# Performance work log

Measured on AMD Instinct MI355X. Metric: run time of the kernel, lower is better.

The kernel has to match this reference:

```python
import jax, jax.numpy as jnp
import numpy as np

N_CAMS, B, J, H, W = 5, 4, 15, 128, 240
CUBE = (80, 80, 20)
NBINS = CUBE[0] * CUBE[1] * CUBE[2]
EPS = 1e-6


def setup_inputs() -> dict:
    key = jax.random.key(0)
    ks = jax.random.split(key, 8)
    heatmaps = jax.random.uniform(ks[0], (N_CAMS, B, J, H, W), dtype=jnp.float32)
    # cameras: rotations about z, placed so scene depth is positive
    ang = np.linspace(0.0, 2 * np.pi, N_CAMS, endpoint=False)
    Rz = np.stack([np.stack([np.cos(ang), -np.sin(ang), np.zeros(N_CAMS)], -1),
                   np.stack([np.sin(ang), np.cos(ang), np.zeros(N_CAMS)], -1),
                   np.stack([np.zeros(N_CAMS), np.zeros(N_CAMS), np.ones(N_CAMS)], -1)], 1)  # [N,3,3]
    R = jnp.asarray(np.broadcast_to(Rz[:, None], (N_CAMS, B, 3, 3)), dtype=jnp.float32)
    T = jnp.broadcast_to(jnp.asarray([0.0, 0.0, -5000.0], jnp.float32), (N_CAMS, B, 3))
    f = jnp.full((N_CAMS, B, 2), 1000.0, jnp.float32)
    c = jnp.broadcast_to(jnp.asarray([960.0, 540.0], jnp.float32), (N_CAMS, B, 2))
    k = 0.01 * jax.random.normal(ks[1], (N_CAMS, B, 3), dtype=jnp.float32)
    p = 0.001 * jax.random.normal(ks[2], (N_CAMS, B, 2), dtype=jnp.float32)
    image_wh = jnp.broadcast_to(jnp.asarray([1920.0, 1080.0], jnp.float32), (N_CAMS, B, 2))
    grid_center = jnp.asarray([0.0, 0.0, 1000.0], jnp.float32) + \
        50.0 * jax.random.normal(ks[3], (B, 3), dtype=jnp.float32)
    grid_size = jnp.asarray([8000.0, 8000.0, 2000.0], jnp.float32)
    return {"heatmaps": heatmaps, "R": R, "T": T, "f": f, "c": c, "k": k,
            "p": p, "image_wh": image_wh, "grid_center": grid_center,
            "grid_size": grid_size}


def compute_grid(grid_size, center):
    # torch.meshgrid default == indexing='ij'
    ax = [jnp.linspace(-grid_size[i] / 2, grid_size[i] / 2, CUBE[i]) + center[i]
          for i in range(3)]
    gx, gy, gz = jnp.meshgrid(ax[0], ax[1], ax[2], indexing='ij')
    return jnp.stack([gx.ravel(), gy.ravel(), gz.ravel()], axis=1)  # [NBINS,3]


def _bilinear_sample(img, g):
    # img [J,H,W]; g [M,2] normalized coords (x,y), align_corners=True, zero pad
    ix = (g[:, 0] + 1.0) * 0.5 * (W - 1)
    iy = (g[:, 1] + 1.0) * 0.5 * (H - 1)
    x0 = jnp.floor(ix); y0 = jnp.floor(iy)
    x1 = x0 + 1.0; y1 = y0 + 1.0
    wx1 = ix - x0; wx0 = 1.0 - wx1
    wy1 = iy - y0; wy0 = 1.0 - wy1

    def gather(xi, yi):
        valid = ((xi >= 0) & (xi < W) & (yi >= 0) & (yi < H)).astype(img.dtype)
        xc = jnp.clip(xi, 0, W - 1).astype(jnp.int32)
        yc = jnp.clip(yi, 0, H - 1).astype(jnp.int32)
        return img[:, yc, xc] * valid  # [J,M]

    return (gather(x0, y0) * (wx0 * wy0) + gather(x1, y0) * (wx1 * wy0) +
            gather(x0, y1) * (wx0 * wy1) + gather(x1, y1) * (wx1 * wy1))


def reference(heatmaps, R, T, f, c, k, p, image_wh, grid_center, grid_size):
    # world grids per sample: [B, NBINS, 3]
    grids = jax.vmap(lambda ctr: compute_grid(grid_size, ctr))(grid_center)
    # project: xcam = R @ (x - T)
    d = grids[None] - T[:, :, None, :]                      # [N,B,M,3]
    xcam = jnp.einsum('nbij,nbmj->nbmi', R, d)              # [N,B,M,3]
    y = xcam[..., :2] / xcam[..., 2:3]                      # [N,B,M,2]
    r2 = jnp.sum(y * y, axis=-1)                            # [N,B,M]
    radial = 1.0 + k[:, :, None, 0] * r2 + k[:, :, None, 1] * r2**2 \
                 + k[:, :, None, 2] * r2**3
    tan = p[:, :, None, 0] * y[..., 1] + p[:, :, None, 1] * y[..., 0]
    xy = y * (radial + tan)[..., None] + \
        r2[..., None] * jnp.stack([p[..., 1], p[..., 0]], -1)[:, :, None, :]
    pix = xy * f[:, :, None, :] + c[:, :, None, :]          # [N,B,M,2]

    wv = image_wh[:, :, None, 0]
    hv = image_wh[:, :, None, 1]
    bound = ((pix[..., 0] >= 0) & (pix[..., 1] >= 0) &
             (pix[..., 0] < wv) & (pix[..., 1] < hv)).astype(heatmaps.dtype)  # [N,B,M]
    maxwh = jnp.maximum(wv, hv)[..., None]
    pixc = jnp.clip(pix, -1.0, maxwh)
    norm = pixc / (image_wh[:, :, None, :] - 1.0) * 2.0 - 1.0
    norm = jnp.clip(norm, -1.1, 1.1)                        # [N,B,M,2]

    sampled = jax.vmap(jax.vmap(_bilinear_sample))(heatmaps, norm)  # [N,B,J,M]

    num = jnp.sum(sampled * bound[:, :, None, :], axis=0)   # [B,J,M]
    den = jnp.sum(bound, axis=0)[:, None, :] + EPS          # [B,1,M]
    cubes = num / den
    cubes = jnp.where(jnp.isnan(cubes), 0.0, cubes)
    cubes = jnp.clip(cubes, 0.0, 1.0)
    cubes = cubes.reshape(B, J, *CUBE)
    return cubes, grids
```

## Files before the change

### kernel.cpp

```cpp
#include <hip/hip_runtime.h>

#define NCAMS 5
#define BB 4
#define JJ 15
#define HH 128
#define WW 240
#define CXX 80
#define CYY 80
#define CZZ 20
#define NBINS 128000
#define HW (HH*WW)
#define CUBES_ELEMS (BB*JJ*NBINS)
#define BLOCK 256
#define BLOCKS_PER_B (NBINS / BLOCK)
#define GRID (BB * BLOCKS_PER_B)
#define WS_NEEDED ((size_t)NCAMS * BB * HW * 16)

__device__ __forceinline__ unsigned prm(unsigned a, unsigned b, unsigned s) {
#if __has_builtin(__builtin_amdgcn_perm)
    return __builtin_amdgcn_perm(a, b, s);
#else
    unsigned long long v = ((unsigned long long)a << 32) | b;
    unsigned r = 0;
#pragma unroll
    for (int i = 0; i < 4; ++i) {
        unsigned idx = (s >> (8 * i)) & 0xffu;
        unsigned byte = (idx < 8) ? (unsigned)((v >> (8 * idx)) & 0xff) : 0u;
        r |= byte << (8 * i);
    }
    return r;
#endif
}

__device__ __forceinline__ unsigned dot4u8(unsigned a, unsigned b, unsigned c) {
#if __has_builtin(__builtin_amdgcn_udot4)
    return __builtin_amdgcn_udot4(a, b, c, false);
#else
    return c + (a & 0xff) * (b & 0xff)
             + ((a >> 8) & 0xff) * ((b >> 8) & 0xff)
             + ((a >> 16) & 0xff) * ((b >> 16) & 0xff)
             + (a >> 24) * (b >> 24);
#endif
}

__global__ __launch_bounds__(BLOCK) void transpose_kernel_u8(
    const float* __restrict__ hm, uint4* __restrict__ tz)
{
    const int t = blockIdx.x * BLOCK + threadIdx.x;
    const int nb = t / HW;
    const int pix = t - nb * HW;
    const float* src = hm + (size_t)nb * JJ * HW + pix;
    unsigned w[4] = {0u, 0u, 0u, 0u};
#pragma unroll
    for (int j = 0; j < JJ; ++j) {
        const float v = src[j * HW];
        unsigned u = (unsigned)(v * 255.f + 0.5f);
        u = u > 255u ? 255u : u;
        w[j >> 2] |= u << ((j & 3) * 8);
    }
    uint4 o; o.x = w[0]; o.y = w[1]; o.z = w[2]; o.w = w[3];
    tz[t] = o;
}

__global__ __launch_bounds__(BLOCK) void project_kernel_u8(
    const uint4* __restrict__ tz,
    const float* __restrict__ R, const float* __restrict__ T,
    const float* __restrict__ f, const float* __restrict__ c,
    const float* __restrict__ k, const float* __restrict__ p,
    const float* __restrict__ wh,
    const float* __restrict__ gc, const float* __restrict__ gs,
    float* __restrict__ out)
{
    const int tile = ((blockIdx.x & 7) * (GRID / 8)) + (blockIdx.x >> 3);
    const int b = tile / BLOCKS_PER_B;
    const int m = (tile % BLOCKS_PER_B) * BLOCK + threadIdx.x;

    const int i   = m / (CYY * CZZ);
    const int rem = m - i * (CYY * CZZ);
    const int jy  = rem / CZZ;
    const int kz  = rem - jy * CZZ;

    const float gs0 = gs[0], gs1 = gs[1], gs2 = gs[2];
    const float gx = -0.5f * gs0 + (float)i  * (gs0 / (float)(CXX - 1)) + gc[b * 3 + 0];
    const float gy = -0.5f * gs1 + (float)jy * (gs1 / (float)(CYY - 1)) + gc[b * 3 + 1];
    const float gz = -0.5f * gs2 + (float)kz * (gs2 / (float)(CZZ - 1)) + gc[b * 3 + 2];

    float* gout = out + CUBES_ELEMS + ((size_t)b * NBINS + m) * 3;
    gout[0] = gx; gout[1] = gy; gout[2] = gz;

    unsigned acc[JJ];
#pragma unroll
    for (int j = 0; j < JJ; ++j) acc[j] = 0u;
    float den = 0.f;

    for (int n = 0; n < NCAMS; ++n) {
        const int pb = n * BB + b;
        const float* Rp = R + pb * 9;

        const float dx = gx - T[pb * 3 + 0];
        const float dy = gy - T[pb * 3 + 1];
        const float dz = gz - T[pb * 3 + 2];

        const float xc = Rp[0] * dx + Rp[1] * dy + Rp[2] * dz;
        const float yc = Rp[3] * dx + Rp[4] * dy + Rp[5] * dz;
        const float zc = Rp[6] * dx + Rp[7] * dy + Rp[8] * dz;

        const float y0 = xc / zc;
        const float y1 = yc / zc;
        const float r2 = y0 * y0 + y1 * y1;

        const float k0 = k[pb * 3 + 0], k1 = k[pb * 3 + 1], k2 = k[pb * 3 + 2];
        const float radial = 1.f + k0 * r2 + k1 * r2 * r2 + k2 * r2 * r2 * r2;
        const float p0v = p[pb * 2 + 0], p1v = p[pb * 2 + 1];
        const float s = radial + p0v * y1 + p1v * y0;
        const float xy0 = y0 * s + r2 * p1v;
        const float xy1 = y1 * s + r2 * p0v;

        const float pixx = xy0 * f[pb * 2 + 0] + c[pb * 2 + 0];
        const float pixy = xy1 * f[pb * 2 + 1] + c[pb * 2 + 1];

        const float wv = wh[pb * 2 + 0], hv = wh[pb * 2 + 1];
        const bool inb = (pixx >= 0.f) & (pixy >= 0.f) & (pixx < wv) & (pixy < hv);
        if (!inb) continue;
        den += 1.f;

        const float maxwh = fmaxf(wv, hv);
        float pcx = fminf(fmaxf(pixx, -1.f), maxwh);
        float pcy = fminf(fmaxf(pixy, -1.f), maxwh);
        float nx = fminf(fmaxf(pcx / (wv - 1.f) * 2.f - 1.f, -1.1f), 1.1f);
        float ny = fminf(fmaxf(pcy / (hv - 1.f) * 2.f - 1.f, -1.1f), 1.1f);

        const float ix = (nx + 1.f) * 0.5f * (float)(WW - 1);
        const float iy = (ny + 1.f) * 0.5f * (float)(HH - 1);
        const float x0f = floorf(ix), y0f = floorf(iy);
        const float x1f = x0f + 1.f, y1f = y0f + 1.f;
        const float wx1 = ix - x0f, wx0 = 1.f - wx1;
        const float wy1 = iy - y0f, wy0 = 1.f - wy1;

        const float vx0 = (x0f >= 0.f && x0f < (float)WW) ? 1.f : 0.f;
        const float vx1 = (x1f >= 0.f && x1f < (float)WW) ? 1.f : 0.f;
        const float vy0 = (y0f >= 0.f && y0f < (float)HH) ? 1.f : 0.f;
        const float vy1 = (y1f >= 0.f && y1f < (float)HH) ? 1.f : 0.f;

        const float w00 = wx0 * wy0 * vx0 * vy0;
        const float w10 = wx1 * wy0 * vx1 * vy0;
        const float w01 = wx0 * wy1 * vx0 * vy1;
        const float w11 = wx1 * wy1 * vx1 * vy1;

        const int xi0 = min(max((int)x0f, 0), WW - 1);
        const int xi1 = min(max((int)x1f, 0), WW - 1);
        const int yi0 = min(max((int)y0f, 0), HH - 1);
        const int yi1 = min(max((int)y1f, 0), HH - 1);

        const uint4* img = tz + (size_t)pb * HW;
        const uint4 A = img[yi0 * WW + xi0];
        const uint4 Bc = img[yi0 * WW + xi1];
        const uint4 Cc = img[yi1 * WW + xi0];
        const uint4 D = img[yi1 * WW + xi1];

        const unsigned u00 = (unsigned)(w00 * 255.f + 0.5f);
        const unsigned u10 = (unsigned)(w10 * 255.f + 0.5f);
        const unsigned u01 = (unsigned)(w01 * 255.f + 0.5f);
        const unsigned u11 = (unsigned)(w11 * 255.f + 0.5f);
        const unsigned wp = u00 | (u10 << 8) | (u01 << 16) | (u11 << 24);

        const unsigned Aa[4] = {A.x,  A.y,  A.z,  A.w};
        const unsigned Ba[4] = {Bc.x, Bc.y, Bc.z, Bc.w};
        const unsigned Ca[4] = {Cc.x, Cc.y, Cc.z, Cc.w};
        const unsigned Da[4] = {D.x,  D.y,  D.z,  D.w};

#pragma unroll
        for (int j = 0; j < JJ; ++j) {
            const int d = j >> 2;
            const unsigned bj = (unsigned)(j & 3);
            const unsigned selAB = 0x0c0c0000u | (bj << 8) | (bj + 4u);
            const unsigned mAB = prm(Aa[d], Ba[d], selAB);
            const unsigned mCD = prm(Ca[d], Da[d], selAB);
            const unsigned bytes = prm(mAB, mCD, 0x01000504u);
            acc[j] = dot4u8(bytes, wp, acc[j]);
        }
    }

    const float inv = 1.f / ((den + 1e-6f) * (255.f * 255.f));
    float* cout = out + (size_t)b * JJ * NBINS + m;
#pragma unroll
    for (int j = 0; j < JJ; ++j) {
        float v = (float)acc[j] * inv;
        v = fminf(fmaxf(v, 0.f), 1.f);
        cout[(size_t)j * NBINS] = v;
    }
}

__global__ __launch_bounds__(BLOCK) void project_kernel_fb(
    const float* __restrict__ hm,
    const float* __restrict__ R, const float* __restrict__ T,
    const float* __restrict__ f, const float* __restrict__ c,
    const float* __restrict__ k, const float* __restrict__ p,
    const float* __restrict__ wh,
    const float* __restrict__ gc, const float* __restrict__ gs,
    float* __restrict__ out)
{
    const int b = blockIdx.x / BLOCKS_PER_B;
    const int m = (blockIdx.x % BLOCKS_PER_B) * BLOCK + threadIdx.x;
    const int i   = m / (CYY * CZZ);
    const int rem = m - i * (CYY * CZZ);
    const int jy  = rem / CZZ;
    const int kz  = rem - jy * CZZ;

    const float gs0 = gs[0], gs1 = gs[1], gs2 = gs[2];
    const float gx = -0.5f * gs0 + (float)i  * (gs0 / (float)(CXX - 1)) + gc[b * 3 + 0];
    const float gy = -0.5f * gs1 + (float)jy * (gs1 / (float)(CYY - 1)) + gc[b * 3 + 1];
    const float gz = -0.5f * gs2 + (float)kz * (gs2 / (float)(CZZ - 1)) + gc[b * 3 + 2];

    float* gout = out + CUBES_ELEMS + ((size_t)b * NBINS + m) * 3;
    gout[0] = gx; gout[1] = gy; gout[2] = gz;

    float num[JJ];
#pragma unroll
    for (int j = 0; j < JJ; ++j) num[j] = 0.f;
    float den = 0.f;

    for (int n = 0; n < NCAMS; ++n) {
        const int pb = n * BB + b;
        const float* Rp = R + pb * 9;
        const float dx = gx - T[pb * 3 + 0];
        const float dy = gy - T[pb * 3 + 1];
        const float dz = gz - T[pb * 3 + 2];
        const float xc = Rp[0] * dx + Rp[1] * dy + Rp[2] * dz;
        const float yc = Rp[3] * dx + Rp[4] * dy + Rp[5] * dz;
        const float zc = Rp[6] * dx + Rp[7] * dy + Rp[8] * dz;
        const float y0 = xc / zc;
        const float y1 = yc / zc;
        const float r2 = y0 * y0 + y1 * y1;
        const float k0 = k[pb * 3 + 0], k1 = k[pb * 3 + 1], k2 = k[pb * 3 + 2];
        const float radial = 1.f + k0 * r2 + k1 * r2 * r2 + k2 * r2 * r2 * r2;
        const float p0v = p[pb * 2 + 0], p1v = p[pb * 2 + 1];
        const float s = radial + p0v * y1 + p1v * y0;
        const float xy0 = y0 * s + r2 * p1v;
        const float xy1 = y1 * s + r2 * p0v;
        const float pixx = xy0 * f[pb * 2 + 0] + c[pb * 2 + 0];
        const float pixy = xy1 * f[pb * 2 + 1] + c[pb * 2 + 1];
        const float wv = wh[pb * 2 + 0], hv = wh[pb * 2 + 1];
        const bool inb = (pixx >= 0.f) & (pixy >= 0.f) & (pixx < wv) & (pixy < hv);
        if (!inb) continue;
        den += 1.f;
        const float maxwh = fmaxf(wv, hv);
        float pcx = fminf(fmaxf(pixx, -1.f), maxwh);
        float pcy = fminf(fmaxf(pixy, -1.f), maxwh);
        float nx = fminf(fmaxf(pcx / (wv - 1.f) * 2.f - 1.f, -1.1f), 1.1f);
        float ny = fminf(fmaxf(pcy / (hv - 1.f) * 2.f - 1.f, -1.1f), 1.1f);
        const float ix = (nx + 1.f) * 0.5f * (float)(WW - 1);
        const float iy = (ny + 1.f) * 0.5f * (float)(HH - 1);
        const float x0f = floorf(ix), y0f = floorf(iy);
        const float x1f = x0f + 1.f, y1f = y0f + 1.f;
        const float wx1 = ix - x0f, wx0 = 1.f - wx1;
        const float wy1 = iy - y0f, wy0 = 1.f - wy1;
        const float vx0 = (x0f >= 0.f && x0f < (float)WW) ? 1.f : 0.f;
        const float vx1 = (x1f >= 0.f && x1f < (float)WW) ? 1.f : 0.f;
        const float vy0 = (y0f >= 0.f && y0f < (float)HH) ? 1.f : 0.f;
        const float vy1 = (y1f >= 0.f && y1f < (float)HH) ? 1.f : 0.f;
        const float w00 = wx0 * wy0 * vx0 * vy0;
        const float w10 = wx1 * wy0 * vx1 * vy0;
        const float w01 = wx0 * wy1 * vx0 * vy1;
        const float w11 = wx1 * wy1 * vx1 * vy1;
        const int xi0 = min(max((int)x0f, 0), WW - 1);
        const int xi1 = min(max((int)x1f, 0), WW - 1);
        const int yi0 = min(max((int)y0f, 0), HH - 1);
        const int yi1 = min(max((int)y1f, 0), HH - 1);
        const int o00 = yi0 * WW + xi0;
        const int o10 = yi0 * WW + xi1;
        const int o01 = yi1 * WW + xi0;
        const int o11 = yi1 * WW + xi1;
        const float* img = hm + (size_t)pb * JJ * HW;
#pragma unroll
        for (int j = 0; j < JJ; ++j) {
            const float* pj = img + j * HW;
            num[j] += pj[o00] * w00 + pj[o10] * w10 + pj[o01] * w01 + pj[o11] * w11;
        }
    }

    const float inv = 1.f / (den + 1e-6f);
    float* cout = out + (size_t)b * JJ * NBINS + m;
#pragma unroll
    for (int j = 0; j < JJ; ++j) {
        float v = num[j] * inv;
        v = (v != v) ? 0.f : v;
        v = fminf(fmaxf(v, 0.f), 1.f);
        cout[(size_t)j * NBINS] = v;
    }
}

extern "C" void kernel_launch(void* const* d_in, const int* in_sizes, int n_in,
                              void* d_out, int out_size, void* d_ws, size_t ws_size,
                              hipStream_t stream) {
    const float* hm = (const float*)d_in[0];
    const float* R  = (const float*)d_in[1];
    const float* T  = (const float*)d_in[2];
    const float* f  = (const float*)d_in[3];
    const float* c  = (const float*)d_in[4];
    const float* k  = (const float*)d_in[5];
    const float* p  = (const float*)d_in[6];
    const float* wh = (const float*)d_in[7];
    const float* gc = (const float*)d_in[8];
    const float* gs = (const float*)d_in[9];
    float* out = (float*)d_out;

    if (ws_size >= WS_NEEDED) {
        uint4* tz = (uint4*)d_ws;
        transpose_kernel_u8<<<dim3(NCAMS * BB * HW / BLOCK), dim3(BLOCK), 0, stream>>>(
            hm, tz);
        project_kernel_u8<<<dim3(GRID), dim3(BLOCK), 0, stream>>>(
            tz, R, T, f, c, k, p, wh, gc, gs, out);
    } else {
        project_kernel_fb<<<dim3(GRID), dim3(BLOCK), 0, stream>>>(
            hm, R, T, f, c, k, p, wh, gc, gs, out);
    }
}
```

Baseline: 119.9 us.

## Use nontemporal memory ops, branchless camera loop, and shared byte-transpose permutes

Heatmap loads in the transpose kernel and the cube and grid output stores now use nontemporal hints, which keeps streaming data from polluting the cache. The camera loop is fully unrolled and made branchless: out-of-bounds cameras zero the packed weights instead of skipping the iteration, which removes divergence but always issues the four gathers. The per-joint 3-permute byte extraction becomes a 4x4 byte transpose per dword that shares intermediate permutes, cutting permute instructions per camera.

```diff
diff --git a/kernel.cpp b/kernel.cpp
--- a/kernel.cpp
+++ b/kernel.cpp
@@ -53,7 +53,7 @@
     unsigned w[4] = {0u, 0u, 0u, 0u};
 #pragma unroll
     for (int j = 0; j < JJ; ++j) {
-        const float v = src[j * HW];
+        const float v = __builtin_nontemporal_load(src + j * HW);
         unsigned u = (unsigned)(v * 255.f + 0.5f);
         u = u > 255u ? 255u : u;
         w[j >> 2] |= u << ((j & 3) * 8);
@@ -86,13 +86,16 @@
     const float gz = -0.5f * gs2 + (float)kz * (gs2 / (float)(CZZ - 1)) + gc[b * 3 + 2];
 
     float* gout = out + CUBES_ELEMS + ((size_t)b * NBINS + m) * 3;
-    gout[0] = gx; gout[1] = gy; gout[2] = gz;
-
-    unsigned acc[JJ];
-#pragma unroll
-    for (int j = 0; j < JJ; ++j) acc[j] = 0u;
+    __builtin_nontemporal_store(gx, gout + 0);
+    __builtin_nontemporal_store(gy, gout + 1);
+    __builtin_nontemporal_store(gz, gout + 2);
+
+    unsigned acc[16];
+#pragma unroll
+    for (int j = 0; j < 16; ++j) acc[j] = 0u;
     float den = 0.f;
 
+#pragma unroll
     for (int n = 0; n < NCAMS; ++n) {
         const int pb = n * BB + b;
         const float* Rp = R + pb * 9;
@@ -121,8 +124,7 @@
 
         const float wv = wh[pb * 2 + 0], hv = wh[pb * 2 + 1];
         const bool inb = (pixx >= 0.f) & (pixy >= 0.f) & (pixx < wv) & (pixy < hv);
-        if (!inb) continue;
-        den += 1.f;
+        den += inb ? 1.f : 0.f;
 
         const float maxwh = fmaxf(wv, hv);
         float pcx = fminf(fmaxf(pixx, -1.f), maxwh);
@@ -153,16 +155,17 @@
         const int yi1 = min(max((int)y1f, 0), HH - 1);
 
         const uint4* img = tz + (size_t)pb * HW;
-        const uint4 A = img[yi0 * WW + xi0];
+        const uint4 A  = img[yi0 * WW + xi0];
         const uint4 Bc = img[yi0 * WW + xi1];
         const uint4 Cc = img[yi1 * WW + xi0];
-        const uint4 D = img[yi1 * WW + xi1];
+        const uint4 D  = img[yi1 * WW + xi1];
 
         const unsigned u00 = (unsigned)(w00 * 255.f + 0.5f);
         const unsigned u10 = (unsigned)(w10 * 255.f + 0.5f);
         const unsigned u01 = (unsigned)(w01 * 255.f + 0.5f);
         const unsigned u11 = (unsigned)(w11 * 255.f + 0.5f);
-        const unsigned wp = u00 | (u10 << 8) | (u01 << 16) | (u11 << 24);
+        unsigned wp = u00 | (u10 << 8) | (u01 << 16) | (u11 << 24);
+        wp = inb ? wp : 0u;
 
         const unsigned Aa[4] = {A.x,  A.y,  A.z,  A.w};
         const unsigned Ba[4] = {Bc.x, Bc.y, Bc.z, Bc.w};
@@ -170,14 +173,19 @@
         const unsigned Da[4] = {D.x,  D.y,  D.z,  D.w};
 
 #pragma unroll
-        for (int j = 0; j < JJ; ++j) {
-            const int d = j >> 2;
-            const unsigned bj = (unsigned)(j & 3);
-            const unsigned selAB = 0x0c0c0000u | (bj << 8) | (bj + 4u);
-            const unsigned mAB = prm(Aa[d], Ba[d], selAB);
-            const unsigned mCD = prm(Ca[d], Da[d], selAB);
-            const unsigned bytes = prm(mAB, mCD, 0x01000504u);
-            acc[j] = dot4u8(bytes, wp, acc[j]);
+        for (int d = 0; d < 4; ++d) {
+            const unsigned tABlo = prm(Aa[d], Ba[d], 0x01050004u);
+            const unsigned tABhi = prm(Aa[d], Ba[d], 0x03070206u);
+            const unsigned tCDlo = prm(Ca[d], Da[d], 0x01050004u);
+            const unsigned tCDhi = prm(Ca[d], Da[d], 0x03070206u);
+            const unsigned r0 = prm(tABlo, tCDlo, 0x01000504u);
+            const unsigned r1 = prm(tABlo, tCDlo, 0x03020706u);
+            const unsigned r2 = prm(tABhi, tCDhi, 0x01000504u);
+            const unsigned r3 = prm(tABhi, tCDhi, 0x03020706u);
+            acc[4 * d + 0] = dot4u8(r0, wp, acc[4 * d + 0]);
+            acc[4 * d + 1] = dot4u8(r1, wp, acc[4 * d + 1]);
+            acc[4 * d + 2] = dot4u8(r2, wp, acc[4 * d + 2]);
+            acc[4 * d + 3] = dot4u8(r3, wp, acc[4 * d + 3]);
         }
     }
 
@@ -187,7 +195,7 @@
     for (int j = 0; j < JJ; ++j) {
         float v = (float)acc[j] * inv;
         v = fminf(fmaxf(v, 0.f), 1.f);
-        cout[(size_t)j * NBINS] = v;
+        __builtin_nontemporal_store(v, cout + (size_t)j * NBINS);
     }
 }
 
```

After: 121.0 us. Within noise of the previous version (+1.0%).
